# Kernel tuning notes

Hardware: AMD Instinct MI355X
Metric: run time of the kernel (lower is better)

Reference implementation:

```python
import jax, jax.numpy as jnp
import numpy as np

ENC = 512   # ENCODER_DIM / card embedding size / LSTM input size
CTX = 512   # context_embeddings width
H = 512     # LSTM hidden size
N = 100000  # num_cards


def _lstm_step(x, h, c, w_ih, w_hh, b_ih, b_hh):
    # PyTorch LSTM gate order: i, f, g, o
    gates = x @ w_ih.T + b_ih + h @ w_hh.T + b_hh
    i, f, g, o = jnp.split(gates, 4, axis=-1)
    c_new = jax.nn.sigmoid(f) * c + jax.nn.sigmoid(i) * jnp.tanh(g)
    h_new = jax.nn.sigmoid(o) * jnp.tanh(c_new)
    return h_new, c_new


def setup_inputs() -> dict:
    key = jax.random.key(0)
    ks = jax.random.split(key, 16)
    s = 0.05
    f32 = jnp.float32
    return {
        "context_embeddings": jax.random.normal(ks[0], (1, CTX), f32),
        "card_embeddings": jax.random.normal(ks[1], (N, ENC), f32),
        "eos_embedding": jax.random.normal(ks[2], (ENC,), f32) * 0.1,
        "ctx_w": jax.random.normal(ks[3], (ENC, CTX), f32) * s,
        "ctx_b": jnp.zeros((ENC,), f32),
        "out_w": jax.random.normal(ks[4], (ENC, H), f32) * s,
        "out_b": jnp.zeros((ENC,), f32),
        "w_ih_0": jax.random.normal(ks[5], (4 * H, ENC), f32) * s,
        "w_hh_0": jax.random.normal(ks[6], (4 * H, H), f32) * s,
        "b_ih_0": jnp.zeros((4 * H,), f32),
        "b_hh_0": jnp.zeros((4 * H,), f32),
        "w_ih_1": jax.random.normal(ks[7], (4 * H, H), f32) * s,
        "w_hh_1": jax.random.normal(ks[8], (4 * H, H), f32) * s,
        "b_ih_1": jnp.zeros((4 * H,), f32),
        "b_hh_1": jnp.zeros((4 * H,), f32),
        "max_selections": 5,
    }


def reference(context_embeddings, card_embeddings, eos_embedding,
              ctx_w, ctx_b, out_w, out_b,
              w_ih_0, w_hh_0, b_ih_0, b_hh_0,
              w_ih_1, w_hh_1, b_ih_1, b_hh_1,
              max_selections):
    temperature = 1.0
    num_cards = card_embeddings.shape[0]
    hid = w_hh_0.shape[1]
    dt = card_embeddings.dtype

    # initial LSTM step on projected context with zero state (seq_len == 1)
    x0 = context_embeddings @ ctx_w.T + ctx_b                     # [1, ENC]
    z = jnp.zeros((1, hid), dt)
    h0, c0 = _lstm_step(x0, z, z, w_ih_0, w_hh_0, b_ih_0, b_hh_0)
    h1, c1 = _lstm_step(h0, z, z, w_ih_1, w_hh_1, b_ih_1, b_hh_1)

    all_emb = jnp.concatenate([card_embeddings, eos_embedding[None, :]], axis=0)  # [N+1, ENC]
    avail = jnp.ones((num_cards,), bool)
    active = jnp.array(True)
    total_log_prob = jnp.asarray(0.0, dt)
    keys = jax.random.split(jax.random.key(42), max_selections)
    card_ids = jnp.arange(num_cards)

    indices = []
    n_steps = min(int(max_selections), num_cards)
    for step in range(n_steps):
        proj = h1 @ out_w.T + out_b                               # [1, ENC]
        card_sims = proj @ card_embeddings.T                      # [1, N]
        eos_sim = proj @ eos_embedding[:, None]                   # [1, 1]
        logits = jnp.concatenate([card_sims, eos_sim], axis=-1)[0] / temperature  # [N+1]
        ext_mask = jnp.concatenate([avail, jnp.ones((1,), bool)])
        logits = jnp.where(ext_mask, logits, -jnp.inf)

        idx = jax.random.categorical(keys[step], logits)          # multinomial(softmax(logits))
        log_prob = jax.nn.log_softmax(logits)[idx]
        total_log_prob = total_log_prob + jnp.where(active, log_prob, jnp.asarray(0.0, dt))

        is_eos = idx == num_cards
        take = active & (~is_eos)
        indices.append(jnp.where(take, idx, -1).astype(jnp.int32))
        avail = avail & ~((card_ids == idx) & take)

        # straight-through one-hot gather of the selected embedding
        hard = jax.nn.one_hot(idx, num_cards + 1, dtype=dt)
        soft = jax.nn.softmax(logits)
        ste = hard + soft - jax.lax.stop_gradient(soft)
        sel_emb = (ste @ all_emb)[None, :]                        # [1, ENC]

        h0, c0 = _lstm_step(sel_emb, h0, c0, w_ih_0, w_hh_0, b_ih_0, b_hh_0)
        h1, c1 = _lstm_step(h0, h1, c1, w_ih_1, w_hh_1, b_ih_1, b_hh_1)
        active = active & (~is_eos)

    selected_indices = jnp.stack(indices)                         # [max_selections], -1 = not selected
    return selected_indices, total_log_prob
```

## Files before the change

### kernel.cpp

```cpp
#include <hip/hip_runtime.h>
#include <stdint.h>
#include <math.h>

#define ENC 512
#define NSTEPS 5
#define NBLK 512
#define NTHR 256
#define NWAVES 2048
#define RPI (NWAVES * 8)
#define NMAST 128
#define GSTRIDE 100032
#define FB_BLOCKS 1024
#define FB_WAVES 4096

#define OFF_SLOT   0
#define OFF_SLOT1  8192
#define OFF_REL1   10240
#define OFF_CFLAG  10752
#define OFF_STEPF  11776
#define OFF_SELS   12800
#define BAR_BYTES  53248

struct SelState {
  int taken[8]; int takenCount; int active; int outIdx[8]; float tlp;
};

struct KParams {
  const float *ctx, *cards, *eos, *ctx_w, *ctx_b, *out_w, *out_b;
  const float *w_ih_0, *w_hh_0, *b_ih_0, *b_hh_0;
  const float *w_ih_1, *w_hh_1, *b_ih_1, *b_hh_1;
  unsigned* bar;
  float* xbuf;
  float* h0s; float* c0s; float* h1s; float* c1s;
  float* projs;
  SelState* st;
  float* bScore; int* bIdxA; float* bLogit; float* bM; float* bS;
  float* gtab;
  float* out;
  int ncards;
  uint32_t k0[NSTEPS], k1[NSTEPS];
};

__host__ __device__ __forceinline__ void tf2x32(uint32_t k0, uint32_t k1,
                                                uint32_t x0, uint32_t x1,
                                                uint32_t& o0, uint32_t& o1) {
  uint32_t ks0 = k0, ks1 = k1, ks2 = k0 ^ k1 ^ 0x1BD11BDAu;
  uint32_t ks[3] = {ks0, ks1, ks2};
  const uint32_t R0[4] = {13u, 15u, 26u, 6u};
  const uint32_t R1[4] = {17u, 29u, 16u, 24u};
  x0 += ks0; x1 += ks1;
#pragma unroll
  for (int i = 0; i < 5; ++i) {
    const uint32_t* r = (i & 1) ? R1 : R0;
#pragma unroll
    for (int j = 0; j < 4; ++j) {
      x0 += x1;
      x1 = (x1 << r[j]) | (x1 >> (32u - r[j]));
      x1 ^= x0;
    }
    x0 += ks[(i + 1) % 3];
    x1 += ks[(i + 2) % 3] + (uint32_t)(i + 1);
  }
  o0 = x0; o1 = x1;
}

__device__ __forceinline__ float gumbel_from_bits(uint32_t bits) {
  float f = __uint_as_float((bits >> 9) | 0x3F800000u) - 1.0f;
  float u = (f == 0.0f) ? 1.17549435e-38f : f;
  return -logf(-logf(u));
}

__device__ __forceinline__ float xla_tanh(float x) {
  if (fabsf(x) < 0.0004f) return x;
  const float kLim = 7.90531110763549805f;
  float cx = fminf(fmaxf(x, -kLim), kLim);
  float x2 = cx * cx;
  float p = -2.76076847742355e-16f;
  p = fmaf(p, x2, 2.00018790482477e-13f);
  p = fmaf(p, x2, -8.60467152213735e-11f);
  p = fmaf(p, x2, 5.12229709037114e-08f);
  p = fmaf(p, x2, 1.48572235717979e-05f);
  p = fmaf(p, x2, 6.37261928875436e-04f);
  p = fmaf(p, x2, 4.89352455891786e-03f);
  p = cx * p;
  float q = 1.19825839466702e-06f;
  q = fmaf(q, x2, 1.18534705686654e-04f);
  q = fmaf(q, x2, 2.26843463243900e-03f);
  q = fmaf(q, x2, 4.89352518554385e-03f);
  return p / q;
}
__device__ __forceinline__ float xla_sigmoid(float x) {
  return 0.5f * xla_tanh(0.5f * x) + 0.5f;
}

__device__ __forceinline__ float dot8(const float4* a, const float4* b, int lane) {
  float4 x0 = a[lane * 2], x1 = a[lane * 2 + 1];
  float4 y0 = b[lane * 2], y1 = b[lane * 2 + 1];
  return x0.x * y0.x + x0.y * y0.y + x0.z * y0.z + x0.w * y0.w +
         x1.x * y1.x + x1.y * y1.y + x1.z * y1.z + x1.w * y1.w;
}
__device__ __forceinline__ float wred(float v) {
#pragma unroll
  for (int k = 1; k < 64; k <<= 1) v += __shfl_xor(v, k, 64);
  return v;
}
__device__ __forceinline__ void cstoref(float* p, float v) {
  __hip_atomic_store(p, v, __ATOMIC_RELAXED, __HIP_MEMORY_SCOPE_AGENT);
}
__device__ __forceinline__ void cstorei(int* p, int v) {
  __hip_atomic_store(p, v, __ATOMIC_RELAXED, __HIP_MEMORY_SCOPE_AGENT);
}
__device__ __forceinline__ unsigned cload(unsigned* p) {
  return __hip_atomic_load(p, __ATOMIC_RELAXED, __HIP_MEMORY_SCOPE_AGENT);
}

__device__ __forceinline__ void arrive_slot(unsigned* slot_base, int idx, unsigned v) {
  asm volatile("s_waitcnt vmcnt(0)" ::: "memory");
  __syncthreads();
  if (threadIdx.x == 0) __hip_atomic_store(&slot_base[(unsigned)idx * 16u], v,
                                           __ATOMIC_RELAXED, __HIP_MEMORY_SCOPE_AGENT);
}
__device__ __forceinline__ void waitfull(unsigned* slots, unsigned v) {
  unsigned* s0 = &slots[(2u * (unsigned)threadIdx.x) * 16u];
  unsigned* s1 = &slots[(2u * (unsigned)threadIdx.x + 1u) * 16u];
  while (cload(s0) < v) __builtin_amdgcn_s_sleep(2);
  while (cload(s1) < v) __builtin_amdgcn_s_sleep(2);
  __syncthreads();
}
__device__ __forceinline__ void wait128(unsigned* slots1, unsigned v) {
  if (threadIdx.x < NMAST) {
    unsigned* s = &slots1[(unsigned)threadIdx.x * 16u];
    while (cload(s) < v) __builtin_amdgcn_s_sleep(1);
  }
  __syncthreads();
}
__device__ __forceinline__ void rel128_set(unsigned* rel1, unsigned v) {
  if (threadIdx.x < 32)
    __hip_atomic_store(&rel1[(unsigned)threadIdx.x * 16u], v,
                       __ATOMIC_RELAXED, __HIP_MEMORY_SCOPE_AGENT);
}
__device__ __forceinline__ void rel128_wait(unsigned* rel1, int bid, unsigned v) {
  if (threadIdx.x == 0) {
    unsigned* r = &rel1[((unsigned)bid & 31u) * 16u];
    while (cload(r) < v) __builtin_amdgcn_s_sleep(1);
  }
  __syncthreads();
}
__device__ __forceinline__ void setflag(unsigned* flag, unsigned v) {
  asm volatile("s_waitcnt vmcnt(0)" ::: "memory");
  __syncthreads();
  if (threadIdx.x < 64)
    __hip_atomic_store(&flag[(unsigned)threadIdx.x * 16u], v,
                       __ATOMIC_RELAXED, __HIP_MEMORY_SCOPE_AGENT);
}
__device__ __forceinline__ void flagwait(unsigned* flag, int bid, unsigned v) {
  if (threadIdx.x == 0) {
    unsigned* r = &flag[((unsigned)bid & 63u) * 16u];
    while (cload(r) < v) __builtin_amdgcn_s_sleep(4);
  }
  __syncthreads();
}

__device__ __forceinline__ void lstm_phase(const float* wih, const float* whh,
                                           const float* bih, const float* bhh,
                                           const float* x, const float* hin, const float* cin,
                                           float* hout, float* cout, float* sG,
                                           int bid, int tid) {
  if (bid < ENC) {
    int g = tid >> 6, lane = tid & 63;
    size_t row = (size_t)(g * ENC + bid) * ENC;
    float accI = dot8((const float4*)(wih + row), (const float4*)x, lane);
    float accH = 0.0f;
    if (hin) accH = dot8((const float4*)(whh + row), (const float4*)hin, lane);
#pragma unroll
    for (int k = 1; k < 64; k <<= 1) {
      accI += __shfl_xor(accI, k, 64);
      accH += __shfl_xor(accH, k, 64);
    }
    if (lane == 0) sG[g] = ((accI + bih[g * ENC + bid]) + accH) + bhh[g * ENC + bid];
    __syncthreads();
    if (tid == 0) {
      float gi = sG[0], gf = sG[1], gg = sG[2], go = sG[3];
      float cprev = cin ? cin[bid] : 0.0f;
      float cn = xla_sigmoid(gf) * cprev + xla_sigmoid(gi) * xla_tanh(gg);
      float hn = xla_sigmoid(go) * xla_tanh(cn);
      cstoref(&cout[bid], cn);
      cstoref(&hout[bid], hn);
    }
  }
}

__global__ __launch_bounds__(NTHR, 2) void mega(KParams P) {
  const int bid = blockIdx.x, tid = threadIdx.x;
  const int wid = tid >> 6, lane = tid & 63;
  const int gw = bid * 4 + wid;
  const int sub = lane & 15, grp = lane >> 4;

  unsigned* slots  = P.bar + OFF_SLOT;
  unsigned* slots1 = P.bar + OFF_SLOT1;
  unsigned* rel1   = P.bar + OFF_REL1;
  unsigned* cflag  = P.bar + OFF_CFLAG;
  unsigned* stepf  = P.bar + OFF_STEPF;
  int*      selS   = (int*)(P.bar + OFF_SELS);

  __shared__ float sGm[4][4];
  __shared__ float fS[NTHR], fL[NTHR], fM[NTHR], fU[NTHR];
  __shared__ int   fI[NTHR];
  __shared__ float wSs[16], wLs[16], wMs[16], wUs[16];
  __shared__ int   wIs[16];
  __shared__ int   tkSh[5];
  __shared__ int   tkCnt;
  __shared__ int   selX;
  __shared__ int   sActive;
  __shared__ float sTlp;
  __shared__ int   sOut[NSTEPS];

  if (tid == 0) {
    tkCnt = 0;
    for (int i = 0; i < 5; ++i) tkSh[i] = -1;
    sActive = 1; sTlp = 0.0f;
    for (int i = 0; i < NSTEPS; ++i) sOut[i] = -1;
  }
  __syncthreads();

  const int np1 = P.ncards + 1;
  const int ITERS = (np1 + RPI - 1) / RPI;

  {
    int s = lane >> 3, k = lane & 7;
    if (s < NSTEPS) {
      for (int t = 0; t < ITERS; ++t) {
        int r = (t * NWAVES + gw) * 8 + k;
        if (r < np1) {
          uint32_t r0, r1;
          tf2x32(P.k0[s], P.k1[s], 0u, (uint32_t)r, r0, r1);
          P.gtab[s * GSTRIDE + r] = gumbel_from_bits(r0 ^ r1);
        }
      }
    }
  }

  auto lstm_cols = [&](const float* wih, const float* whh,
                       const float* bih, const float* bhh,
                       const float* x, const float* hin, const float* cin,
                       float* hout, float* cout) {
    const float4* xv = (const float4*)x;
    float4 xa = xv[lane * 2], xb = xv[lane * 2 + 1];
    float4 ha, hb;
    if (hin) {
      const float4* hv = (const float4*)hin;
      ha = hv[lane * 2]; hb = hv[lane * 2 + 1];
    }
    for (int j = 0; j < 4; ++j) {
      int col = bid * 4 + j;
      size_t row = (size_t)(wid * ENC + col) * ENC;
      const float4* wi = (const float4*)(wih + row);
      float4 a0 = wi[lane * 2], a1 = wi[lane * 2 + 1];
      float accI = a0.x * xa.x + a0.y * xa.y + a0.z * xa.z + a0.w * xa.w +
                   a1.x * xb.x + a1.y * xb.y + a1.z * xb.z + a1.w * xb.w;
      float accH = 0.0f;
      if (hin) {
        const float4* wh = (const float4*)(whh + row);
        float4 b0 = wh[lane * 2], b1 = wh[lane * 2 + 1];
        accH = b0.x * ha.x + b0.y * ha.y + b0.z * ha.z + b0.w * ha.w +
               b1.x * hb.x + b1.y * hb.y + b1.z * hb.z + b1.w * hb.w;
      }
#pragma unroll
      for (int k = 1; k < 64; k <<= 1) {
        accI += __shfl_xor(accI, k, 64);
        accH += __shfl_xor(accH, k, 64);
      }
      if (lane == 0) sGm[wid][j] = ((accI + bih[wid * ENC + col]) + accH) + bhh[wid * ENC + col];
    }
    __syncthreads();
    if (tid < 4) {
      int col = bid * 4 + tid;
      float gi = sGm[0][tid], gf = sGm[1][tid], gg = sGm[2][tid], go = sGm[3][tid];
      float cprev = cin ? cin[col] : 0.0f;
      float cn = xla_sigmoid(gf) * cprev + xla_sigmoid(gi) * xla_tanh(gg);
      float hn = xla_sigmoid(go) * xla_tanh(cn);
      cstoref(&cout[col], cn);
      cstoref(&hout[col], hn);
    }
    __syncthreads();
  };
  auto proj_phase = [&](const float* h1, float* dst) {
    const float4* ow = (const float4*)(P.out_w + (size_t)gw * ENC);
    float acc = wred(dot8(ow, (const float4*)h1, lane));
    if (lane == 0) cstoref(&dst[gw], acc + P.out_b[gw]);
  };

  unsigned b128 = 0;
  if (bid < NMAST) {
    {
      const float4* cw = (const float4*)(P.ctx_w + (size_t)gw * ENC);
      float acc = wred(dot8(cw, (const float4*)P.ctx, lane));
      if (lane == 0) cstoref(&P.xbuf[gw], acc + P.ctx_b[gw]);
    }
    arrive_slot(slots1, bid, ++b128);
    if (bid == 0) { wait128(slots1, b128); rel128_set(rel1, b128); }
    else rel128_wait(rel1, bid, b128);
    if (bid == 0) __syncthreads();

    lstm_cols(P.w_ih_0, P.w_hh_0, P.b_ih_0, P.b_hh_0, P.xbuf, nullptr, nullptr, P.h0s, P.c0s);
    arrive_slot(slots1, bid, ++b128);
    if (bid == 0) { wait128(slots1, b128); rel128_set(rel1, b128); }
    else rel128_wait(rel1, bid, b128);
    if (bid == 0) __syncthreads();

    lstm_cols(P.w_ih_1, P.w_hh_1, P.b_ih_1, P.b_hh_1, P.h0s, nullptr, nullptr, P.h1s, P.c1s);
    arrive_slot(slots1, bid, ++b128);
    if (bid == 0) { wait128(slots1, b128); rel128_set(rel1, b128); }
    else rel128_wait(rel1, bid, b128);
    if (bid == 0) __syncthreads();

    proj_phase(P.h1s, P.projs);
    arrive_slot(slots1, bid, ++b128);
    if (bid == 0) { wait128(slots1, b128); setflag(stepf, 1); }
  } else {
    b128 = 4;
  }
  flagwait(stepf, bid, 1);

  for (int s = 0; s < NSTEPS; ++s) {
    {
      const float4* pv = (const float4*)(P.projs + s * ENC);
      float4 pr[8];
#pragma unroll
      for (int k = 0; k < 8; ++k) pr[k] = pv[sub + 16 * k];
      int t0 = tkSh[0], t1 = tkSh[1], t2 = tkSh[2], t3 = tkSh[3], t4 = tkSh[4];
      const float* gt = P.gtab + s * GSTRIDE;
      float bSc = -INFINITY, bLg = 0.0f, m = -INFINITY, su = 0.0f;
      int bIx = 0x7FFFFFFF;
      for (int t = 0; t < ITERS; ++t) {
        int base = (t * NWAVES + gw) * 8;
        int rA = base + grp;
        int rB = base + 4 + grp;
        bool vA = (rA < np1), vB = (rB < np1);
        const float* rpA = vA ? ((rA < P.ncards) ? (P.cards + (size_t)rA * ENC) : P.eos) : P.cards;
        const float* rpB = vB ? ((rB < P.ncards) ? (P.cards + (size_t)rB * ENC) : P.eos) : P.cards;
        const float4* ra = (const float4*)rpA;
        const float4* rb = (const float4*)rpB;
        float4 rrA[8], rrB[8];
#pragma unroll
        for (int k = 0; k < 8; ++k) { rrA[k] = ra[sub + 16 * k]; rrB[k] = rb[sub + 16 * k]; }
        float gA = vA ? gt[rA] : 0.0f;
        float gB = vB ? gt[rB] : 0.0f;
        float accA = 0.0f, accB = 0.0f;
#pragma unroll
        for (int k = 0; k < 8; ++k) {
          accA += rrA[k].x * pr[k].x + rrA[k].y * pr[k].y + rrA[k].z * pr[k].z + rrA[k].w * pr[k].w;
          accB += rrB[k].x * pr[k].x + rrB[k].y * pr[k].y + rrB[k].z * pr[k].z + rrB[k].w * pr[k].w;
        }
        accA += __shfl_xor(accA, 1, 64); accB += __shfl_xor(accB, 1, 64);
        accA += __shfl_xor(accA, 2, 64); accB += __shfl_xor(accB, 2, 64);
        accA += __shfl_xor(accA, 4, 64); accB += __shfl_xor(accB, 4, 64);
        accA += __shfl_xor(accA, 8, 64); accB += __shfl_xor(accB, 8, 64);
        if (sub == 0) {
          if (vA) {
            bool masked = (rA < P.ncards) &&
                          (rA == t0 || rA == t1 || rA == t2 || rA == t3 || rA == t4);
            if (!masked) {
              if (accA > m) { su = su * expf(m - accA) + 1.0f; m = accA; }
              else          { su += expf(accA - m); }
              float score = gA + accA;
              if (score > bSc || (score == bSc && rA < bIx)) { bSc = score; bIx = rA; bLg = accA; }
            }
          }
          if (vB) {
            bool masked = (rB < P.ncards) &&
                          (rB == t0 || rB == t1 || rB == t2 || rB == t3 || rB == t4);
            if (!masked) {
              if (accB > m) { su = su * expf(m - accB) + 1.0f; m = accB; }
              else          { su += expf(accB - m); }
              float score = gB + accB;
              if (score > bSc || (score == bSc && rB < bIx)) { bSc = score; bIx = rB; bLg = accB; }
            }
          }
        }
      }
      if (sub == 0) {
        int q = wid * 4 + grp;
        wSs[q] = bSc; wIs[q] = bIx; wLs[q] = bLg; wMs[q] = m; wUs[q] = su;
      }
      __syncthreads();
      if (tid == 0) {
        float s2 = wSs[0], l2 = wLs[0], m2 = wMs[0], u2 = wUs[0];
        int i2 = wIs[0];
        for (int k = 1; k < 16; ++k) {
          float cs = wSs[k]; int ci = wIs[k];
          if (cs > s2 || (cs == s2 && ci < i2)) { s2 = cs; i2 = ci; l2 = wLs[k]; }
          float cm = wMs[k], cu = wUs[k];
          if (cm > m2) { u2 = u2 * expf(m2 - cm) + cu; m2 = cm; }
          else if (cm > -INFINITY) { u2 += cu * expf(cm - m2); }
        }
        int o = s * NBLK + bid;
        cstoref(&P.bScore[o], s2); cstorei(&P.bIdxA[o], i2);
        cstoref(&P.bLogit[o], l2); cstoref(&P.bM[o], m2); cstoref(&P.bS[o], u2);
      }
    }
    arrive_slot(slots, bid, (unsigned)(s + 1));
    if (s == NSTEPS - 1 && bid != 0) return;

    if (bid == 0) {
      waitfull(slots, (unsigned)(s + 1));
      const float* pSc = P.bScore + s * NBLK;
      const int*   pIx = P.bIdxA  + s * NBLK;
      const float* pLg = P.bLogit + s * NBLK;
      const float* pMm = P.bM     + s * NBLK;
      const float* pSu = P.bS     + s * NBLK;
      float bS2 = -INFINITY, bL2 = 0.0f, m = -INFINITY, su = 0.0f;
      int bI2 = 0x7FFFFFFF;
      for (int i = tid; i < NBLK; i += NTHR) {
        float cs = pSc[i]; int ci = pIx[i];
        if (cs > bS2 || (cs == bS2 && ci < bI2)) { bS2 = cs; bI2 = ci; bL2 = pLg[i]; }
        float cm = pMm[i], cu = pSu[i];
        if (cm > m) { su = su * expf(m - cm) + cu; m = cm; }
        else if (cm > -INFINITY) { su += cu * expf(cm - m); }
      }
      fS[tid] = bS2; fI[tid] = bI2; fL[tid] = bL2; fM[tid] = m; fU[tid] = su;
      __syncthreads();
      for (int off = 128; off > 0; off >>= 1) {
        if (tid < off) {
          float cs = fS[tid + off]; int ci = fI[tid + off];
          if (cs > fS[tid] || (cs == fS[tid] && ci < fI[tid])) {
            fS[tid] = cs; fI[tid] = ci; fL[tid] = fL[tid + off];
          }
          float cm = fM[tid + off], cu = fU[tid + off];
          if (cm > fM[tid]) { fU[tid] = fU[tid] * expf(fM[tid] - cm) + cu; fM[tid] = cm; }
          else if (cm > -INFINITY) { fU[tid] += cu * expf(cm - fM[tid]); }
        }
        __syncthreads();
      }
      if (tid == 0) {
        int idx = fI[0];
        float lse = fM[0] + logf(fU[0]);
        float lp = fL[0] - lse;
        int active = sActive;
        if (active) sTlp += lp;
        int is_eos = (idx == P.ncards);
        int take = active && !is_eos;
        sOut[s] = take ? idx : -1;
        sActive = active && !is_eos;
        if (s == NSTEPS - 1) {
          for (int q = 0; q < NSTEPS; ++q) P.out[q] = (float)sOut[q];
          P.out[NSTEPS] = sTlp;
        } else {
          cstorei(&selS[s * 16], idx);
          cstorei(&selS[s * 16 + 1], take ? idx : -1);
        }
      }
      __syncthreads();
      if (s == NSTEPS - 1) return;
      setflag(cflag, (unsigned)(s + 1));
    }

    if (bid < NMAST) {
      flagwait(cflag, bid, (unsigned)(s + 1));
      if (tid == 0) {
        int xI = selS[s * 16];
        int tI = selS[s * 16 + 1];
        selX = xI;
        if (tI >= 0) tkSh[tkCnt++] = tI;
      }
      __syncthreads();
      {
        int idx = selX;
        const float* xrow = (idx < P.ncards) ? (P.cards + (size_t)idx * ENC) : P.eos;
        lstm_cols(P.w_ih_0, P.w_hh_0, P.b_ih_0, P.b_hh_0, xrow,
                  P.h0s + s * ENC, P.c0s + s * ENC,
                  P.h0s + (s + 1) * ENC, P.c0s + (s + 1) * ENC);
      }
      arrive_slot(slots1, bid, ++b128);
      if (bid == 0) { wait128(slots1, b128); rel128_set(rel1, b128); }
      else rel128_wait(rel1, bid, b128);
      if (bid == 0) __syncthreads();

      lstm_cols(P.w_ih_1, P.w_hh_1, P.b_ih_1, P.b_hh_1, P.h0s + (s + 1) * ENC,
                P.h1s + s * ENC, P.c1s + s * ENC,
                P.h1s + (s + 1) * ENC, P.c1s + (s + 1) * ENC);
      arrive_slot(slots1, bid, ++b128);
      if (bid == 0) { wait128(slots1, b128); rel128_set(rel1, b128); }
      else rel128_wait(rel1, bid, b128);
      if (bid == 0) __syncthreads();

      proj_phase(P.h1s + (s + 1) * ENC, P.projs + (s + 1) * ENC);
      arrive_slot(slots1, bid, ++b128);
      if (bid == 0) { wait128(slots1, b128); setflag(stepf, (unsigned)(s + 2)); }
      flagwait(stepf, bid, (unsigned)(s + 2));
    } else {
      b128 += 3;
      flagwait(stepf, bid, (unsigned)(s + 2));
      if (tid == 0) {
        int tI = selS[s * 16 + 1];
        if (tI >= 0) tkSh[tkCnt++] = tI;
      }
      __syncthreads();
    }
  }
}

__global__ void init_kernel(float* __restrict__ Z, SelState* st) {
  int t = threadIdx.x;
  if (t < ENC) Z[t] = 0.0f;
  if (t == 0) {
    for (int i = 0; i < 8; ++i) { st->taken[i] = -1; st->outIdx[i] = -1; }
    st->takenCount = 0; st->active = 1; st->tlp = 0.0f;
  }
}

__global__ void gumbel_fill(float* __restrict__ gtab, int ncards,
                            uint32_t k00, uint32_t k01, uint32_t k10, uint32_t k11,
                            uint32_t k20, uint32_t k21, uint32_t k30, uint32_t k31,
                            uint32_t k40, uint32_t k41) {
  uint32_t K0[NSTEPS] = {k00, k10, k20, k30, k40};
  uint32_t K1[NSTEPS] = {k01, k11, k21, k31, k41};
  int np1 = ncards + 1;
  int total = NSTEPS * np1;
  for (int j = blockIdx.x * blockDim.x + threadIdx.x; j < total; j += gridDim.x * blockDim.x) {
    int s = j / np1;
    int i = j - s * np1;
    uint32_t r0, r1;
    tf2x32(K0[s], K1[s], 0u, (uint32_t)i, r0, r1);
    gtab[s * GSTRIDE + i] = gumbel_from_bits(r0 ^ r1);
  }
}

__global__ void matvec512(const float* __restrict__ W, const float* __restrict__ b,
                          const float* __restrict__ vin, float* __restrict__ vout) {
  int tid = blockIdx.x * blockDim.x + threadIdx.x;
  int wave = tid >> 6, lane = tid & 63;
  if (wave >= ENC) return;
  float acc = wred(dot8((const float4*)(W + (size_t)wave * ENC), (const float4*)vin, lane));
  if (lane == 0) vout[wave] = acc + b[wave];
}

__global__ void lstm_step_kernel(const float* __restrict__ w_ih, const float* __restrict__ w_hh,
                                 const float* __restrict__ b_ih, const float* __restrict__ b_hh,
                                 const float* __restrict__ x, const float* __restrict__ h_in,
                                 const float* __restrict__ c_in,
                                 float* __restrict__ h_out, float* __restrict__ c_out) {
  __shared__ float sG[4];
  lstm_phase(w_ih, w_hh, b_ih, b_hh, x, h_in, c_in, h_out, c_out, sG,
             blockIdx.x, threadIdx.x);
}

__global__ void sims_kernel(const float* __restrict__ cards, const float* __restrict__ eos,
                            const float* __restrict__ proj, int ncards,
                            const float* __restrict__ gt,
                            const int* __restrict__ takenList,
                            float* __restrict__ oScore, int* __restrict__ oIdx,
                            float* __restrict__ oLogit, float* __restrict__ oM,
                            float* __restrict__ oS) {
  int tid = blockIdx.x * blockDim.x + threadIdx.x;
  int wave = tid >> 6, lane = tid & 63;
  int nwav = (gridDim.x * blockDim.x) >> 6;
  const float4* pv = (const float4*)proj;
  float4 p0 = pv[lane * 2], p1 = pv[lane * 2 + 1];
  int t0 = takenList[0], t1 = takenList[1], t2 = takenList[2],
      t3 = takenList[3], t4 = takenList[4];
  float bS = -INFINITY, bL = 0.0f, m = -INFINITY, s = 0.0f;
  int bI = 0x7FFFFFFF;
  for (int i = wave; i <= ncards; i += nwav) {
    const float* rowp = (i < ncards) ? (cards + (size_t)i * ENC) : eos;
    const float4* er = (const float4*)rowp;
    float4 e0 = er[lane * 2], e1 = er[lane * 2 + 1];
    float acc = p0.x * e0.x + p0.y * e0.y + p0.z * e0.z + p0.w * e0.w +
                p1.x * e1.x + p1.y * e1.y + p1.z * e1.z + p1.w * e1.w;
    acc = wred(acc);
    bool masked = (i < ncards) &&
                  (i == t0 || i == t1 || i == t2 || i == t3 || i == t4);
    if (!masked) {
      if (acc > m) { s = s * expf(m - acc) + 1.0f; m = acc; }
      else         { s += expf(acc - m); }
      float score = gt[i] + acc;
      if (score > bS || (score == bS && i < bI)) { bS = score; bI = i; bL = acc; }
    }
  }
  if (lane == 0) { oScore[wave] = bS; oIdx[wave] = bI; oLogit[wave] = bL; oM[wave] = m; oS[wave] = s; }
}

__global__ void finalize_kernel(int nw, int step, int ncards,
                                const float* __restrict__ pScore, const int* __restrict__ pIdx,
                                const float* __restrict__ pLogit, const float* __restrict__ pM,
                                const float* __restrict__ pS,
                                const float* __restrict__ cards, const float* __restrict__ eos,
                                SelState* st, float* __restrict__ xout,
                                float* __restrict__ out, int write_out) {
  __shared__ float sS[256], sL[256], sM[256], sU[256];
  __shared__ int sI[256];
  __shared__ int selIdx;
  int t = threadIdx.x;
  float bS = -INFINITY, bL = 0.0f, m = -INFINITY, s = 0.0f;
  int bI = 0x7FFFFFFF;
  for (int i = t; i < nw; i += 256) {
    float cs = pScore[i]; int ci = pIdx[i];
    if (cs > bS || (cs == bS && ci < bI)) { bS = cs; bI = ci; bL = pLogit[i]; }
    float cm = pM[i], cu = pS[i];
    if (cm > m) { s = s * expf(m - cm) + cu; m = cm; }
    else if (cm > -INFINITY) { s += cu * expf(cm - m); }
  }
  sS[t] = bS; sI[t] = bI; sL[t] = bL; sM[t] = m; sU[t] = s;
  __syncthreads();
  for (int off = 128; off > 0; off >>= 1) {
    if (t < off) {
      float cs = sS[t + off]; int ci = sI[t + off];
      if (cs > sS[t] || (cs == sS[t] && ci < sI[t])) { sS[t] = cs; sI[t] = ci; sL[t] = sL[t + off]; }
      float cm = sM[t + off], cu = sU[t + off];
      if (cm > sM[t]) { sU[t] = sU[t] * expf(sM[t] - cm) + cu; sM[t] = cm; }
      else if (cm > -INFINITY) { sU[t] += cu * expf(cm - sM[t]); }
    }
    __syncthreads();
  }
  if (t == 0) {
    int idx = sI[0];
    float lse = sM[0] + logf(sU[0]);
    float lp = sL[0] - lse;
    int active = st->active;
    if (active) st->tlp += lp;
    int is_eos = (idx == ncards);
    int take = active && !is_eos;
    st->outIdx[step] = take ? idx : -1;
    if (take) st->taken[st->takenCount++] = idx;
    st->active = active && !is_eos;
    selIdx = idx;
    if (write_out) {
      for (int q = 0; q < NSTEPS; ++q) out[q] = (float)st->outIdx[q];
      out[NSTEPS] = st->tlp;
    }
  }
  __syncthreads();
  if (!write_out) {
    int idx = selIdx;
    const float* row = (idx < ncards) ? (cards + (size_t)idx * ENC) : eos;
    for (int e = t; e < ENC; e += 256) xout[e] = row[e];
  }
}

extern "C" void kernel_launch(void* const* d_in, const int* in_sizes, int n_in,
                              void* d_out, int out_size, void* d_ws, size_t ws_size,
                              hipStream_t stream) {
  KParams P;
  P.ctx    = (const float*)d_in[0];
  P.cards  = (const float*)d_in[1];
  P.eos    = (const float*)d_in[2];
  P.ctx_w  = (const float*)d_in[3];
  P.ctx_b  = (const float*)d_in[4];
  P.out_w  = (const float*)d_in[5];
  P.out_b  = (const float*)d_in[6];
  P.w_ih_0 = (const float*)d_in[7];
  P.w_hh_0 = (const float*)d_in[8];
  P.b_ih_0 = (const float*)d_in[9];
  P.b_hh_0 = (const float*)d_in[10];
  P.w_ih_1 = (const float*)d_in[11];
  P.w_hh_1 = (const float*)d_in[12];
  P.b_ih_1 = (const float*)d_in[13];
  P.b_hh_1 = (const float*)d_in[14];
  P.ncards = in_sizes[1] / ENC;

  char* wsb = (char*)d_ws;
  P.bar = (unsigned*)wsb;
  float* f = (float*)(wsb + BAR_BYTES);
  float* Z = f; f += ENC;
  P.xbuf = f; f += ENC;
  P.h0s = f; f += 6 * ENC;
  P.c0s = f; f += 6 * ENC;
  P.h1s = f; f += 6 * ENC;
  P.c1s = f; f += 6 * ENC;
  P.projs = f; f += NSTEPS * ENC;
  P.st = (SelState*)f;  f = (float*)((char*)f + 256);
  P.bScore = f; f += FB_WAVES;
  P.bIdxA = (int*)f; f += FB_WAVES;
  P.bLogit = f; f += FB_WAVES;
  P.bM = f; f += FB_WAVES;
  P.bS = f; f += FB_WAVES;
  P.gtab = f;
  P.out = (float*)d_out;

  for (int s = 0; s < NSTEPS; ++s)
    tf2x32(0u, 42u, 0u, (uint32_t)s, P.k0[s], P.k1[s]);

  hipMemsetAsync(P.bar, 0, BAR_BYTES, stream);

  void* args[] = { &P };
  hipError_t ce = hipLaunchCooperativeKernel((void*)mega, dim3(NBLK), dim3(NTHR), args, 0, stream);
  if (ce == hipSuccess) return;
  (void)hipGetLastError();

  float* h0A = P.h0s;            float* h0B = P.h0s + ENC;
  float* c0A = P.c0s;            float* c0B = P.c0s + ENC;
  float* h1A = P.h1s;            float* h1B = P.h1s + ENC;
  float* c1A = P.c1s;            float* c1B = P.c1s + ENC;
  float* proj = P.projs;
  float* xbuf = P.xbuf;

  init_kernel<<<1, 512, 0, stream>>>(Z, P.st);
  gumbel_fill<<<512, 256, 0, stream>>>(P.gtab, P.ncards,
                                       P.k0[0], P.k1[0], P.k0[1], P.k1[1], P.k0[2], P.k1[2],
                                       P.k0[3], P.k1[3], P.k0[4], P.k1[4]);
  matvec512<<<128, 256, 0, stream>>>(P.ctx_w, P.ctx_b, P.ctx, xbuf);
  lstm_step_kernel<<<512, 256, 0, stream>>>(P.w_ih_0, P.w_hh_0, P.b_ih_0, P.b_hh_0,
                                            xbuf, Z, Z, h0A, c0A);
  lstm_step_kernel<<<512, 256, 0, stream>>>(P.w_ih_1, P.w_hh_1, P.b_ih_1, P.b_hh_1,
                                            h0A, Z, Z, h1A, c1A);
  float *h0c = h0A, *c0c = c0A, *h1c = h1A, *c1c = c1A;
  float *h0n = h0B, *c0n = c0B, *h1n = h1B, *c1n = c1B;
  for (int s = 0; s < NSTEPS; ++s) {
    matvec512<<<128, 256, 0, stream>>>(P.out_w, P.out_b, h1c, proj);
    sims_kernel<<<FB_BLOCKS, 256, 0, stream>>>(P.cards, P.eos, proj, P.ncards,
                                               P.gtab + s * GSTRIDE, (const int*)P.st,
                                               P.bScore, P.bIdxA, P.bLogit, P.bM, P.bS);
    finalize_kernel<<<1, 256, 0, stream>>>(FB_WAVES, s, P.ncards,
                                           P.bScore, P.bIdxA, P.bLogit, P.bM, P.bS,
                                           P.cards, P.eos, P.st, xbuf,
                                           P.out, (s == NSTEPS - 1) ? 1 : 0);
    if (s == NSTEPS - 1) break;
    lstm_step_kernel<<<512, 256, 0, stream>>>(P.w_ih_0, P.w_hh_0, P.b_ih_0, P.b_hh_0,
                                              xbuf, h0c, c0c, h0n, c0n);
    lstm_step_kernel<<<512, 256, 0, stream>>>(P.w_ih_1, P.w_hh_1, P.b_ih_1, P.b_hh_1,
                                              h0n, h1c, c1c, h1n, c1n);
    float* tp;
    tp = h0c; h0c = h0n; h0n = tp;
    tp = c0c; c0c = c0n; c0n = tp;
    tp = h1c; h1c = h1n; h1n = tp;
    tp = c1c; c1c = c1n; c1n = tp;
  }
}
```

Baseline: 303.5 us.

## Double block size to 512 threads and halve LSTM master blocks to 64

```diff
diff --git a/kernel.cpp b/kernel.cpp
--- a/kernel.cpp
+++ b/kernel.cpp
@@ -5,21 +5,22 @@
 #define ENC 512
 #define NSTEPS 5
 #define NBLK 512
-#define NTHR 256
-#define NWAVES 2048
+#define NTHR 512
+#define WPB 8
+#define NWAVES (NBLK * WPB)
 #define RPI (NWAVES * 8)
-#define NMAST 128
+#define NMAST 64
 #define GSTRIDE 100032
 #define FB_BLOCKS 1024
 #define FB_WAVES 4096
 
 #define OFF_SLOT   0
 #define OFF_SLOT1  8192
-#define OFF_REL1   10240
-#define OFF_CFLAG  10752
-#define OFF_STEPF  11776
-#define OFF_SELS   12800
-#define BAR_BYTES  53248
+#define OFF_REL1   9216
+#define OFF_CFLAG  9728
+#define OFF_STEPF  10752
+#define OFF_SELS   11776
+#define BAR_BYTES  49152
 
 struct SelState {
   int taken[8]; int takenCount; int active; int outIdx[8]; float tlp;
@@ -113,38 +114,15 @@
 __device__ __forceinline__ unsigned cload(unsigned* p) {
   return __hip_atomic_load(p, __ATOMIC_RELAXED, __HIP_MEMORY_SCOPE_AGENT);
 }
+__device__ __forceinline__ int iload(int* p) {
+  return __hip_atomic_load(p, __ATOMIC_RELAXED, __HIP_MEMORY_SCOPE_AGENT);
+}
 
 __device__ __forceinline__ void arrive_slot(unsigned* slot_base, int idx, unsigned v) {
   asm volatile("s_waitcnt vmcnt(0)" ::: "memory");
   __syncthreads();
   if (threadIdx.x == 0) __hip_atomic_store(&slot_base[(unsigned)idx * 16u], v,
                                            __ATOMIC_RELAXED, __HIP_MEMORY_SCOPE_AGENT);
-}
-__device__ __forceinline__ void waitfull(unsigned* slots, unsigned v) {
-  unsigned* s0 = &slots[(2u * (unsigned)threadIdx.x) * 16u];
-  unsigned* s1 = &slots[(2u * (unsigned)threadIdx.x + 1u) * 16u];
-  while (cload(s0) < v) __builtin_amdgcn_s_sleep(2);
-  while (cload(s1) < v) __builtin_amdgcn_s_sleep(2);
-  __syncthreads();
-}
-__device__ __forceinline__ void wait128(unsigned* slots1, unsigned v) {
-  if (threadIdx.x < NMAST) {
-    unsigned* s = &slots1[(unsigned)threadIdx.x * 16u];
-    while (cload(s) < v) __builtin_amdgcn_s_sleep(1);
-  }
-  __syncthreads();
-}
-__device__ __forceinline__ void rel128_set(unsigned* rel1, unsigned v) {
-  if (threadIdx.x < 32)
-    __hip_atomic_store(&rel1[(unsigned)threadIdx.x * 16u], v,
-                       __ATOMIC_RELAXED, __HIP_MEMORY_SCOPE_AGENT);
-}
-__device__ __forceinline__ void rel128_wait(unsigned* rel1, int bid, unsigned v) {
-  if (threadIdx.x == 0) {
-    unsigned* r = &rel1[((unsigned)bid & 31u) * 16u];
-    while (cload(r) < v) __builtin_amdgcn_s_sleep(1);
-  }
-  __syncthreads();
 }
 __device__ __forceinline__ void setflag(unsigned* flag, unsigned v) {
   asm volatile("s_waitcnt vmcnt(0)" ::: "memory");
@@ -190,10 +168,10 @@
   }
 }
 
-__global__ __launch_bounds__(NTHR, 2) void mega(KParams P) {
+__global__ __launch_bounds__(NTHR, 4) void mega(KParams P) {
   const int bid = blockIdx.x, tid = threadIdx.x;
   const int wid = tid >> 6, lane = tid & 63;
-  const int gw = bid * 4 + wid;
+  const int gw = bid * WPB + wid;
   const int sub = lane & 15, grp = lane >> 4;
 
   unsigned* slots  = P.bar + OFF_SLOT;
@@ -203,11 +181,11 @@
   unsigned* stepf  = P.bar + OFF_STEPF;
   int*      selS   = (int*)(P.bar + OFF_SELS);
 
-  __shared__ float sGm[4][4];
+  __shared__ float sGm[4][8];
   __shared__ float fS[NTHR], fL[NTHR], fM[NTHR], fU[NTHR];
   __shared__ int   fI[NTHR];
-  __shared__ float wSs[16], wLs[16], wMs[16], wUs[16];
-  __shared__ int   wIs[16];
+  __shared__ float wSs[32], wLs[32], wMs[32], wUs[32];
+  __shared__ int   wIs[32];
   __shared__ int   tkSh[5];
   __shared__ int   tkCnt;
   __shared__ int   selX;
@@ -240,10 +218,10 @@
     }
   }
 
-  auto lstm_cols = [&](const float* wih, const float* whh,
-                       const float* bih, const float* bhh,
-                       const float* x, const float* hin, const float* cin,
-                       float* hout, float* cout) {
+  auto lstm_cols8 = [&](const float* wih, const float* whh,
+                        const float* bih, const float* bhh,
+                        const float* x, const float* hin, const float* cin,
+                        float* hout, float* cout) {
     const float4* xv = (const float4*)x;
     float4 xa = xv[lane * 2], xb = xv[lane * 2 + 1];
     float4 ha, hb;
@@ -251,9 +229,10 @@
       const float4* hv = (const float4*)hin;
       ha = hv[lane * 2]; hb = hv[lane * 2 + 1];
     }
+    int gate = wid & 3, half = wid >> 2;
     for (int j = 0; j < 4; ++j) {
-      int col = bid * 4 + j;
-      size_t row = (size_t)(wid * ENC + col) * ENC;
+      int col = bid * 8 + half * 4 + j;
+      size_t row = (size_t)(gate * ENC + col) * ENC;
       const float4* wi = (const float4*)(wih + row);
       float4 a0 = wi[lane * 2], a1 = wi[lane * 2 + 1];
       float accI = a0.x * xa.x + a0.y * xa.y + a0.z * xa.z + a0.w * xa.w +
@@ -270,11 +249,12 @@
         accI += __shfl_xor(accI, k, 64);
         accH += __shfl_xor(accH, k, 64);
       }
-      if (lane == 0) sGm[wid][j] = ((accI + bih[wid * ENC + col]) + accH) + bhh[wid * ENC + col];
+      if (lane == 0)
+        sGm[gate][half * 4 + j] = ((accI + bih[gate * ENC + col]) + accH) + bhh[gate * ENC + col];
     }
     __syncthreads();
-    if (tid < 4) {
-      int col = bid * 4 + tid;
+    if (tid < 8) {
+      int col = bid * 8 + tid;
       float gi = sGm[0][tid], gf = sGm[1][tid], gg = sGm[2][tid], go = sGm[3][tid];
       float cprev = cin ? cin[col] : 0.0f;
       float cn = xla_sigmoid(gf) * cprev + xla_sigmoid(gi) * xla_tanh(gg);
@@ -285,42 +265,59 @@
     __syncthreads();
   };
   auto proj_phase = [&](const float* h1, float* dst) {
-    const float4* ow = (const float4*)(P.out_w + (size_t)gw * ENC);
-    float acc = wred(dot8(ow, (const float4*)h1, lane));
-    if (lane == 0) cstoref(&dst[gw], acc + P.out_b[gw]);
+    if (gw < ENC) {
+      const float4* ow = (const float4*)(P.out_w + (size_t)gw * ENC);
+      float acc = wred(dot8(ow, (const float4*)h1, lane));
+      if (lane == 0) cstoref(&dst[gw], acc + P.out_b[gw]);
+    }
   };
-
-  unsigned b128 = 0;
+  auto mbar = [&](unsigned v) {
+    arrive_slot(slots1, bid, v);
+    if (bid == 0) {
+      if (tid < NMAST) {
+        unsigned* s = &slots1[(unsigned)tid * 16u];
+        while (cload(s) < v) __builtin_amdgcn_s_sleep(1);
+      }
+      __syncthreads();
+      if (tid < 32)
+        __hip_atomic_store(&rel1[(unsigned)tid * 16u], v,
+                           __ATOMIC_RELAXED, __HIP_MEMORY_SCOPE_AGENT);
+      __syncthreads();
+    } else {
+      if (tid == 0) {
+        unsigned* r = &rel1[((unsigned)bid & 31u) * 16u];
+        while (cload(r) < v) __builtin_amdgcn_s_sleep(1);
+      }
+      __syncthreads();
+    }
+  };
+
+  unsigned mb = 0;
   if (bid < NMAST) {
-    {
+    if (gw < ENC) {
       const float4* cw = (const float4*)(P.ctx_w + (size_t)gw * ENC);
       float acc = wred(dot8(cw, (const float4*)P.ctx, lane));
       if (lane == 0) cstoref(&P.xbuf[gw], acc + P.ctx_b[gw]);
     }
-    arrive_slot(slots1, bid, ++b128);
-    if (bid == 0) { wait128(slots1, b128); rel128_set(rel1, b128); }
-    else rel128_wait(rel1, bid, b128);
-    if (bid == 0) __syncthreads();
-
-    lstm_cols(P.w_ih_0, P.w_hh_0, P.b_ih_0, P.b_hh_0, P.xbuf, nullptr, nullptr, P.h0s, P.c0s);
-    arrive_slot(slots1, bid, ++b128);
-    if (bid == 0) { wait128(slots1, b128); rel128_set(rel1, b128); }
-    else rel128_wait(rel1, bid, b128);
-    if (bid == 0) __syncthreads();
-
-    lstm_cols(P.w_ih_1, P.w_hh_1, P.b_ih_1, P.b_hh_1, P.h0s, nullptr, nullptr, P.h1s, P.c1s);
-    arrive_slot(slots1, bid, ++b128);
-    if (bid == 0) { wait128(slots1, b128); rel128_set(rel1, b128); }
-    else rel128_wait(rel1, bid, b128);
-    if (bid == 0) __syncthreads();
-
+    mbar(++mb);
+    lstm_cols8(P.w_ih_0, P.w_hh_0, P.b_ih_0, P.b_hh_0, P.xbuf, nullptr, nullptr, P.h0s, P.c0s);
+    mbar(++mb);
+    lstm_cols8(P.w_ih_1, P.w_hh_1, P.b_ih_1, P.b_hh_1, P.h0s, nullptr, nullptr, P.h1s, P.c1s);
+    mbar(++mb);
     proj_phase(P.h1s, P.projs);
-    arrive_slot(slots1, bid, ++b128);
-    if (bid == 0) { wait128(slots1, b128); setflag(stepf, 1); }
+    arrive_slot(slots1, bid, ++mb);
+    if (bid == 0) {
+      if (tid < NMAST) {
+        unsigned* s = &slots1[(unsigned)tid * 16u];
+        while (cload(s) < mb) __builtin_amdgcn_s_sleep(1);
+      }
+      __syncthreads();
+      setflag(stepf, 1u);
+    }
   } else {
-    b128 = 4;
-  }
-  flagwait(stepf, bid, 1);
+    mb = 4;
+  }
+  flagwait(stepf, bid, 1u);
 
   for (int s = 0; s < NSTEPS; ++s) {
     {
@@ -387,7 +384,7 @@
       if (tid == 0) {
         float s2 = wSs[0], l2 = wLs[0], m2 = wMs[0], u2 = wUs[0];
         int i2 = wIs[0];
-        for (int k = 1; k < 16; ++k) {
+        for (int k = 1; k < 32; ++k) {
           float cs = wSs[k]; int ci = wIs[k];
           if (cs > s2 || (cs == s2 && ci < i2)) { s2 = cs; i2 = ci; l2 = wLs[k]; }
           float cm = wMs[k], cu = wUs[k];
@@ -403,24 +400,20 @@
     if (s == NSTEPS - 1 && bid != 0) return;
 
     if (bid == 0) {
-      waitfull(slots, (unsigned)(s + 1));
+      {
+        unsigned* sl = &slots[(unsigned)tid * 16u];
+        while (cload(sl) < (unsigned)(s + 1)) __builtin_amdgcn_s_sleep(2);
+      }
+      __syncthreads();
       const float* pSc = P.bScore + s * NBLK;
       const int*   pIx = P.bIdxA  + s * NBLK;
       const float* pLg = P.bLogit + s * NBLK;
       const float* pMm = P.bM     + s * NBLK;
       const float* pSu = P.bS     + s * NBLK;
-      float bS2 = -INFINITY, bL2 = 0.0f, m = -INFINITY, su = 0.0f;
-      int bI2 = 0x7FFFFFFF;
-      for (int i = tid; i < NBLK; i += NTHR) {
-        float cs = pSc[i]; int ci = pIx[i];
-        if (cs > bS2 || (cs == bS2 && ci < bI2)) { bS2 = cs; bI2 = ci; bL2 = pLg[i]; }
-        float cm = pMm[i], cu = pSu[i];
-        if (cm > m) { su = su * expf(m - cm) + cu; m = cm; }
-        else if (cm > -INFINITY) { su += cu * expf(cm - m); }
-      }
-      fS[tid] = bS2; fI[tid] = bI2; fL[tid] = bL2; fM[tid] = m; fU[tid] = su;
-      __syncthreads();
-      for (int off = 128; off > 0; off >>= 1) {
+      fS[tid] = pSc[tid]; fI[tid] = pIx[tid]; fL[tid] = pLg[tid];
+      fM[tid] = pMm[tid]; fU[tid] = pSu[tid];
+      __syncthreads();
+      for (int off = 256; off > 0; off >>= 1) {
         if (tid < off) {
           float cs = fS[tid + off]; int ci = fI[tid + off];
           if (cs > fS[tid] || (cs == fS[tid] && ci < fI[tid])) {
@@ -446,8 +439,8 @@
           for (int q = 0; q < NSTEPS; ++q) P.out[q] = (float)sOut[q];
           P.out[NSTEPS] = sTlp;
         } else {
-          cstorei(&selS[s * 16], idx);
-          cstorei(&selS[s * 16 + 1], take ? idx : -1);
+          cstorei(&selS[s * 32], idx);
+          cstorei(&selS[s * 32 + 1], take ? idx : -1);
         }
       }
       __syncthreads();
@@ -458,8 +451,8 @@
     if (bid < NMAST) {
       flagwait(cflag, bid, (unsigned)(s + 1));
       if (tid == 0) {
-        int xI = selS[s * 16];
-        int tI = selS[s * 16 + 1];
+        int xI = iload(&selS[s * 32]);
+        int tI = iload(&selS[s * 32 + 1]);
         selX = xI;
         if (tI >= 0) tkSh[tkCnt++] = tI;
       }
@@ -467,32 +460,31 @@
       {
         int idx = selX;
         const float* xrow = (idx < P.ncards) ? (P.cards + (size_t)idx * ENC) : P.eos;
-        lstm_cols(P.w_ih_0, P.w_hh_0, P.b_ih_0, P.b_hh_0, xrow,
-                  P.h0s + s * ENC, P.c0s + s * ENC,
-                  P.h0s + (s + 1) * ENC, P.c0s + (s + 1) * ENC);
-      }
-      arrive_slot(slots1, bid, ++b128);
-      if (bid == 0) { wait128(slots1, b128); rel128_set(rel1, b128); }
-      else rel128_wait(rel1, bid, b128);
-      if (bid == 0) __syncthreads();
-
-      lstm_cols(P.w_ih_1, P.w_hh_1, P.b_ih_1, P.b_hh_1, P.h0s + (s + 1) * ENC,
-                P.h1s + s * ENC, P.c1s + s * ENC,
-                P.h1s + (s + 1) * ENC, P.c1s + (s + 1) * ENC);
-      arrive_slot(slots1, bid, ++b128);
-      if (bid == 0) { wait128(slots1, b128); rel128_set(rel1, b128); }
-      else rel128_wait(rel1, bid, b128);
-      if (bid == 0) __syncthreads();
-
+        lstm_cols8(P.w_ih_0, P.w_hh_0, P.b_ih_0, P.b_hh_0, xrow,
+                   P.h0s + s * ENC, P.c0s + s * ENC,
+                   P.h0s + (s + 1) * ENC, P.c0s + (s + 1) * ENC);
+      }
+      mbar(++mb);
+      lstm_cols8(P.w_ih_1, P.w_hh_1, P.b_ih_1, P.b_hh_1, P.h0s + (s + 1) * ENC,
+                 P.h1s + s * ENC, P.c1s + s * ENC,
+                 P.h1s + (s + 1) * ENC, P.c1s + (s + 1) * ENC);
+      mbar(++mb);
       proj_phase(P.h1s + (s + 1) * ENC, P.projs + (s + 1) * ENC);
-      arrive_slot(slots1, bid, ++b128);
-      if (bid == 0) { wait128(slots1, b128); setflag(stepf, (unsigned)(s + 2)); }
+      arrive_slot(slots1, bid, ++mb);
+      if (bid == 0) {
+        if (tid < NMAST) {
+          unsigned* sl = &slots1[(unsigned)tid * 16u];
+          while (cload(sl) < mb) __builtin_amdgcn_s_sleep(1);
+        }
+        __syncthreads();
+        setflag(stepf, (unsigned)(s + 2));
+      }
       flagwait(stepf, bid, (unsigned)(s + 2));
     } else {
-      b128 += 3;
+      mb += 3;
       flagwait(stepf, bid, (unsigned)(s + 2));
       if (tid == 0) {
-        int tI = selS[s * 16 + 1];
+        int tI = iload(&selS[s * 32 + 1]);
         if (tI >= 0) tkSh[tkCnt++] = tI;
       }
       __syncthreads();
```

New measurement: 434.2 us. 43.0% more time.
